# Optimization experiments

Measured on AMD Instinct MI355X. Metric: run time of the kernel, lower is better.

## Reference

```python
import jax, jax.numpy as jnp
import numpy as np

B, T, N, DIN, HID, ED, K = 64, 12, 1024, 2, 64, 10, 2

def setup_inputs() -> dict:
    key = jax.random.key(0)
    ks = jax.random.split(key, 18)
    g = lambda i, shape, s=0.1: jax.random.normal(ks[i], shape, jnp.float32) * s
    return dict(
        x=g(0, (B, T, N, DIN), 1.0),
        node_embeddings=g(1, (N, ED), 1.0),
        # GCRN cell 0 (dim_in=DIN): gate -> 2*HID, update -> HID
        Wg0=g(2, (ED, K, DIN + HID, 2 * HID)), bg0=g(3, (ED, 2 * HID)),
        Wu0=g(4, (ED, K, DIN + HID, HID)),     bu0=g(5, (ED, HID)),
        # GCRN cell 1 (dim_in=HID)
        Wg1=g(6, (ED, K, 2 * HID, 2 * HID)),   bg1=g(7, (ED, 2 * HID)),
        Wu1=g(8, (ED, K, 2 * HID, HID)),       bu1=g(9, (ED, HID)),
        # RelatinoShipConv: pointwise Linear(input_dim -> rnn_units), torch [out,in]
        Wr=g(10, (HID, DIN)), br=g(11, (HID,)),
        # end_conv1: Linear(HID,HID, bias=False) (num_layers>1 branch)
        W1=g(12, (HID, HID)),
        # self.conv: Conv2d(horizon, horizon, (1, HID+1), bias=False), OIHW
        Wc=g(13, (T, T, 1, HID + 1)),
        # end_conv2: Conv2d(horizon, horizon, (1, HID), bias)
        W2=g(14, (T, T, 1, HID)), b2=g(15, (T,)),
        # end_conv3: Conv2d(horizon, horizon, (1, 2), dilation (1, HID), bias)
        W3=g(16, (T, T, 1, 2)), b3=g(17, (T,)),
    )

def _avwgcn(x, supports, E, Wp, bp):
    # x:[B,N,C], supports:[K,N,N], E:[N,ED] -> [B,N,O]  (AGCRN adaptive graph conv)
    xg = jnp.einsum('knm,bmc->bnkc', supports, x)
    W = jnp.einsum('ne,ekio->nkio', E, Wp)
    b = E @ bp
    return jnp.einsum('bnki,nkio->bno', xg, W) + b

def _cell(xt, h, supports, E, Wg, bg, Wu, bu):
    # GCRN GRU cell
    zr = jax.nn.sigmoid(_avwgcn(jnp.concatenate([xt, h], -1), supports, E, Wg, bg))
    z, r = jnp.split(zr, 2, -1)
    hc = jnp.tanh(_avwgcn(jnp.concatenate([xt, z * h], -1), supports, E, Wu, bu))
    return r * h + (1.0 - r) * hc

def _conv2d(x, w, b=None, rhs_dilation=(1, 1)):
    y = jax.lax.conv_general_dilated(x, w, (1, 1), 'VALID',
        rhs_dilation=rhs_dilation, dimension_numbers=('NCHW', 'OIHW', 'NCHW'))
    return y if b is None else y + b[None, :, None, None]

def _forward(x, E, Wg0, bg0, Wu0, bu0, Wg1, bg1, Wu1, bu1, Wr, br, W1, Wc, W2, b2, W3, b3):
    A = jax.nn.softmax(jax.nn.relu(E @ E.T), axis=1)
    supports = jnp.stack([jnp.eye(N, dtype=x.dtype), A], 0)  # [K,N,N]
    # GCRN encoder: python loop over 2 layers, lax.scan over the 12 timesteps
    cur = x
    for (Wg, bg, Wu, bu) in ((Wg0, bg0, Wu0, bu0), (Wg1, bg1, Wu1, bu1)):
        h0 = jnp.zeros((x.shape[0], N, HID), x.dtype)
        def step(h, xt):
            h = _cell(xt, h, supports, E, Wg, bg, Wu, bu)
            return h, h
        _, hs = jax.lax.scan(step, h0, jnp.swapaxes(cur, 0, 1))
        cur = jnp.swapaxes(hs, 0, 1)  # [B,T,N,HID]
    out = cur @ W1.T  # end_conv1 (Linear, no bias); dropout is identity in eval
    relation = x @ Wr.T + br  # [B,T,N,HID]
    # torch einsum 'btnc,knn->kbcnt' takes the DIAGONAL of supports over n
    rg = jnp.einsum('btnc,knn->kbcnt', relation, supports)
    rg = jnp.transpose(rg, (1, 4, 3, 2, 0)).reshape(x.shape[0], T, N, -1)  # [B,12,N,2*HID]
    rst = _conv2d(rg, Wc)  # [B,12,N,HID]
    out = _conv2d(jnp.concatenate([rst, out], -1), W2, b2)  # [B,12,N,HID+1]
    out = _conv2d(out, W3, b3, rhs_dilation=(1, HID))       # [B,12,N,1]
    return out

def reference(x, node_embeddings, Wg0, bg0, Wu0, bu0, Wg1, bg1, Wu1, bu1, Wr, br, W1, Wc, W2, b2, W3, b3):
    return _forward(x, node_embeddings, Wg0, bg0, Wu0, bu0, Wg1, bg1, Wu1, bu1, Wr, br, W1, Wc, W2, b2, W3, b3)
```

## Files before the change

kernel.cpp:

```cpp
#include <hip/hip_runtime.h>

typedef unsigned short u16;
typedef unsigned int   u32;

__device__ __forceinline__ float bf2f(u16 u){ return __uint_as_float(((u32)u)<<16); }
__device__ __forceinline__ u16 f2bf(float f){
  u32 u = __float_as_uint(f);
  return (u16)((u + 0x7fffu + ((u>>16)&1u)) >> 16);
}

__global__ __launch_bounds__(256) void k_A2(const float* __restrict__ E,
    float* __restrict__ A, float* __restrict__ diagA)
{
  __shared__ float EL[10][1024];
  __shared__ float row[1024];
  __shared__ float red[4];
  int n = blockIdx.x, tid = threadIdx.x;
  for (int idx=tid; idx<10240; idx+=256)
    EL[idx>>10][idx&1023] = E[(idx&1023)*10 + (idx>>10)];
  __syncthreads();
  float en[10];
#pragma unroll
  for (int e=0;e<10;++e) en[e] = EL[e][n];
  float lmax = -1e30f;
#pragma unroll
  for (int j=0;j<4;++j){
    int m = tid*4 + j;
    float d = 0.f;
#pragma unroll
    for (int e=0;e<10;++e) d = fmaf(en[e], EL[e][m], d);
    d = fmaxf(d, 0.f);
    row[m] = d; lmax = fmaxf(lmax, d);
  }
#pragma unroll
  for (int o=32;o>0;o>>=1) lmax = fmaxf(lmax, __shfl_xor(lmax, o));
  if ((tid&63)==0) red[tid>>6] = lmax;
  __syncthreads();
  float mx = fmaxf(fmaxf(red[0],red[1]), fmaxf(red[2],red[3]));
  __syncthreads();
  float lsum = 0.f;
#pragma unroll
  for (int j=0;j<4;++j){
    int m = tid*4 + j;
    float ex = expf(row[m] - mx);
    row[m] = ex; lsum += ex;
  }
#pragma unroll
  for (int o=32;o>0;o>>=1) lsum += __shfl_xor(lsum, o);
  if ((tid&63)==0) red[tid>>6] = lsum;
  __syncthreads();
  float inv = 1.f/(red[0]+red[1]+red[2]+red[3]);
#pragma unroll
  for (int j=0;j<4;++j){
    int m = tid*4 + j;
    float v = row[m]*inv;
    A[(size_t)n*1024 + m] = v;
    if (m == n) diagA[n] = v;
  }
}

__global__ __launch_bounds__(64) void k_b3eff(
    const float* __restrict__ b2, const float* __restrict__ W3,
    const float* __restrict__ b3, float* __restrict__ b3eff)
{
  int o = threadIdx.x;
  if (o < 12){
    float a = b3[o];
    for (int i=0;i<12;++i)
      a += b2[i] * (W3[(o*12+i)*2] + W3[(o*12+i)*2+1]);
    b3eff[o] = a;
  }
}

__global__ __launch_bounds__(256) void k_Vpre(const float* __restrict__ W1,
    const float* __restrict__ W2, float* __restrict__ V)
{
  int idx = blockIdx.x*256 + threadIdx.x;
  if (idx >= 9216) return;
  int c = idx & 63, r = idx >> 6;
  int j = r % 12, i = r / 12;
  float a = 0.f;
  for (int o=0;o<64;++o)
    a = fmaf(W2[(i*12+j)*64+o], W1[o*64+c], a);
  V[idx] = a;
}

__global__ __launch_bounds__(256) void k_Gpre(const float* __restrict__ Wc,
    const float* __restrict__ W2, u16* __restrict__ G)
{
  int idx = blockIdx.x*256 + threadIdx.x;
  int u = idx & 127, r = idx >> 7;
  int ip = r % 12, i = r / 12;
  float a = 0.f;
  int wlo = u>64 ? u-64 : 0;
  int whi = u<63 ? u : 63;
  for (int j=0;j<12;++j){
    const float* w2r = W2 + (i*12+j)*64;
    const float* wcr = Wc + (j*12+ip)*65;
    for (int w=wlo; w<=whi; ++w)
      a = fmaf(w2r[w], wcr[u-w], a);
  }
  G[idx] = f2bf(a);
}

__global__ __launch_bounds__(256) void gemm3f(const float* __restrict__ A,
    const float* __restrict__ X, float* __restrict__ Y)
{
  int n0 = blockIdx.x * 128;
  long base = (long)blockIdx.y * 65536;
  __shared__ float At[16][132];
  __shared__ float Xt[16][64];
  int tid = threadIdx.x;
  int tx = tid & 15, ty = tid >> 4;
  float acc[8][4];
#pragma unroll
  for (int r=0;r<8;++r){ acc[r][0]=0;acc[r][1]=0;acc[r][2]=0;acc[r][3]=0; }

  for (int m0=0; m0<1024; m0+=16){
    {
      int r = tid>>1, kh = (tid&1)*8;
      const float* ap = A + (size_t)(n0+r)*1024 + m0 + kh;
      float4 q0 = *(const float4*)ap;
      float4 q1 = *(const float4*)(ap+4);
      At[kh+0][r]=q0.x; At[kh+1][r]=q0.y; At[kh+2][r]=q0.z; At[kh+3][r]=q0.w;
      At[kh+4][r]=q1.x; At[kh+5][r]=q1.y; At[kh+6][r]=q1.z; At[kh+7][r]=q1.w;
    }
    {
      int c = tid & 63, kq = tid >> 6;
#pragma unroll
      for (int j=0;j<4;++j)
        Xt[kq*4+j][c] = X[base + (long)(m0+kq*4+j)*64 + c];
    }
    __syncthreads();
#pragma unroll
    for (int kk=0;kk<16;++kk){
      float4 xv = *(const float4*)&Xt[kk][tx*4];
      float4 a0 = *(const float4*)&At[kk][ty*4];
      float4 a1 = *(const float4*)&At[kk][64+ty*4];
      float av[8] = {a0.x,a0.y,a0.z,a0.w,a1.x,a1.y,a1.z,a1.w};
      float xw[4] = {xv.x,xv.y,xv.z,xv.w};
#pragma unroll
      for (int r=0;r<8;++r)
#pragma unroll
        for (int c=0;c<4;++c) acc[r][c] = fmaf(av[r], xw[c], acc[r][c]);
    }
    __syncthreads();
  }
#pragma unroll
  for (int half=0; half<2; ++half)
#pragma unroll
    for (int i=0;i<4;++i){
      int row = n0 + half*64 + ty*4 + i;
      float4 v; v.x=acc[half*4+i][0]; v.y=acc[half*4+i][1];
      v.z=acc[half*4+i][2]; v.w=acc[half*4+i][3];
      *(float4*)&Y[base + (long)row*64 + tx*4] = v;
    }
}

__global__ __launch_bounds__(256) void gemm2x(const float* __restrict__ A,
    const float* __restrict__ x, float* __restrict__ Y)
{
  __shared__ float As[64][65];
  __shared__ float Xs[64][65];
  int n0 = blockIdx.x*64;
  int q0 = blockIdx.y*64;
  int tid = threadIdx.x, c = tid & 63, rq = tid >> 6;
  float acc[16];
#pragma unroll
  for (int j=0;j<16;++j) acc[j]=0.f;
  for (int m0=0; m0<1024; m0+=64){
#pragma unroll
    for (int j=0;j<16;++j){
      int idx = tid + j*256;
      int r = idx>>6, k = idx&63;
      As[r][k] = A[(size_t)(n0+r)*1024 + m0 + k];
      int qg = q0 + k;
      Xs[r][k] = x[(size_t)(qg>>1)*2048 + (size_t)(m0+r)*2 + (qg&1)];
    }
    __syncthreads();
    for (int k=0;k<64;++k){
      float xv = Xs[k][c];
#pragma unroll
      for (int j=0;j<16;++j) acc[j] = fmaf(As[rq+4*j][k], xv, acc[j]);
    }
    __syncthreads();
  }
#pragma unroll
  for (int j=0;j<16;++j)
    Y[(size_t)(n0+rq+4*j)*1536 + q0 + c] = acc[j];
}

template<int L>
__global__ __launch_bounds__(256) void k_gate2(
    const float* __restrict__ Wg, const float* __restrict__ bgp,
    const float* __restrict__ E,
    const float* __restrict__ xsrc, const float* __restrict__ Axt,
    const float* __restrict__ h, const float* __restrict__ Ah,
    float* __restrict__ zh, float* __restrict__ rb, int t, int first)
{
  constexpr int IX  = (L==0)?2:64;
  constexpr int KI  = 2*(IX+64);
  constexpr int CH  = (L==0)?44:32;
  constexpr int NCH = KI/CH;
  constexpr int O   = 128;
  __shared__ float inp[32][KI];
  __shared__ float Wl[CH][O];
  __shared__ float En[10];
  int n = blockIdx.x, b0 = blockIdx.y*32, tid = threadIdx.x;

  if (tid < 10) En[tid] = E[n*10 + tid];
  for (int idx=tid; idx<32*IX; idx+=256){
    int bl = idx/IX, i = idx - bl*IX; int b = b0+bl;
    inp[bl][i] = (L==0)
      ? xsrc[(size_t)((b*12+t)*1024+n)*2 + i]
      : xsrc[((size_t)b<<16) + (size_t)n*64 + i];
  }
  for (int idx=tid; idx<2048; idx+=256){
    int bl = idx>>6, c = idx&63; int b = b0+bl;
    inp[bl][IX+c] = first ? 0.f : h[((size_t)b<<16) + (size_t)n*64 + c];
  }
  for (int idx=tid; idx<32*IX; idx+=256){
    int bl = idx/IX, i = idx - bl*IX; int b = b0+bl;
    inp[bl][IX+64+i] = (L==0)
      ? Axt[(size_t)n*1536 + (size_t)(b*12+t)*2 + i]
      : Axt[((size_t)b<<16) + (size_t)n*64 + i];
  }
  for (int idx=tid; idx<2048; idx+=256){
    int bl = idx>>6, c = idx&63; int b = b0+bl;
    inp[bl][2*IX+64+c] = first ? 0.f : Ah[((size_t)b<<16) + (size_t)n*64 + c];
  }
  __syncthreads();

  int bg = tid >> 5;
  int og = tid & 31;
  float acc[4][4];
#pragma unroll
  for (int d=0;d<4;++d){
    int o = og*4+d;
    float a = 0.f;
#pragma unroll
    for (int e=0;e<10;++e) a = fmaf(En[e], bgp[e*O+o], a);
#pragma unroll
    for (int bl=0;bl<4;++bl) acc[bl][d] = a;
  }

  for (int ch=0; ch<NCH; ++ch){
    for (int idx=tid; idx<CH*O; idx+=256){
      int i = idx>>7, o = idx&127;
      float a = 0.f;
#pragma unroll
      for (int e=0;e<10;++e)
        a = fmaf(En[e], Wg[((size_t)e*KI + ch*CH + i)*O + o], a);
      Wl[i][o] = a;
    }
    __syncthreads();
    for (int i=0; i<CH; i+=4){
      float4 xq[4], wq[4];
#pragma unroll
      for (int bl=0;bl<4;++bl) xq[bl] = *(const float4*)&inp[bg*4+bl][ch*CH+i];
#pragma unroll
      for (int ii=0;ii<4;++ii) wq[ii] = *(const float4*)&Wl[i+ii][og*4];
      float xv[4][4], wv[4][4];
#pragma unroll
      for (int bl=0;bl<4;++bl){ xv[bl][0]=xq[bl].x; xv[bl][1]=xq[bl].y; xv[bl][2]=xq[bl].z; xv[bl][3]=xq[bl].w; }
#pragma unroll
      for (int ii=0;ii<4;++ii){ wv[ii][0]=wq[ii].x; wv[ii][1]=wq[ii].y; wv[ii][2]=wq[ii].z; wv[ii][3]=wq[ii].w; }
#pragma unroll
      for (int bl=0;bl<4;++bl)
#pragma unroll
        for (int d=0;d<4;++d)
#pragma unroll
          for (int ii=0;ii<4;++ii)
            acc[bl][d] = fmaf(xv[bl][ii], wv[ii][d], acc[bl][d]);
    }
    __syncthreads();
  }

#pragma unroll
  for (int bl=0;bl<4;++bl){
    int b = b0 + bg*4 + bl;
    size_t base = ((size_t)b<<16) + (size_t)n*64;
#pragma unroll
    for (int d=0;d<4;++d){
      int o = og*4 + d;
      float s = 1.f/(1.f+__expf(-acc[bl][d]));
      if (o < 64){
        if (!first) zh[base+o] = s * h[base+o];
      } else {
        rb[base+o-64] = s;
      }
    }
  }
}

template<int L>
__global__ __launch_bounds__(256) void k_upd2(
    const float* __restrict__ Wu, const float* __restrict__ bup,
    const float* __restrict__ E,
    const float* __restrict__ xsrc, const float* __restrict__ Axt,
    const float* __restrict__ zh, const float* __restrict__ Azh,
    const float* __restrict__ rb, float* __restrict__ h, int t, int first)
{
  constexpr int IX  = (L==0)?2:64;
  constexpr int KI  = 2*(IX+64);
  constexpr int CH  = (L==0)?44:64;
  constexpr int NCH = KI/CH;
  constexpr int O   = 64;
  __shared__ float inp[32][KI];
  __shared__ float Wl[CH][O];
  __shared__ float En[10];
  int n = blockIdx.x, b0 = blockIdx.y*32, tid = threadIdx.x;

  if (tid < 10) En[tid] = E[n*10 + tid];
  for (int idx=tid; idx<32*IX; idx+=256){
    int bl = idx/IX, i = idx - bl*IX; int b = b0+bl;
    inp[bl][i] = (L==0)
      ? xsrc[(size_t)((b*12+t)*1024+n)*2 + i]
      : xsrc[((size_t)b<<16) + (size_t)n*64 + i];
  }
  for (int idx=tid; idx<2048; idx+=256){
    int bl = idx>>6, c = idx&63; int b = b0+bl;
    inp[bl][IX+c] = first ? 0.f : zh[((size_t)b<<16) + (size_t)n*64 + c];
  }
  for (int idx=tid; idx<32*IX; idx+=256){
    int bl = idx/IX, i = idx - bl*IX; int b = b0+bl;
    inp[bl][IX+64+i] = (L==0)
      ? Axt[(size_t)n*1536 + (size_t)(b*12+t)*2 + i]
      : Axt[((size_t)b<<16) + (size_t)n*64 + i];
  }
  for (int idx=tid; idx<2048; idx+=256){
    int bl = idx>>6, c = idx&63; int b = b0+bl;
    inp[bl][2*IX+64+c] = first ? 0.f : Azh[((size_t)b<<16) + (size_t)n*64 + c];
  }
  __syncthreads();

  int bg = tid >> 5;
  int og = tid & 31;
  float acc[4][2];
#pragma unroll
  for (int d=0;d<2;++d){
    int o = og*2+d;
    float a = 0.f;
#pragma unroll
    for (int e=0;e<10;++e) a = fmaf(En[e], bup[e*O+o], a);
#pragma unroll
    for (int bl=0;bl<4;++bl) acc[bl][d] = a;
  }

  for (int ch=0; ch<NCH; ++ch){
    for (int idx=tid; idx<CH*O; idx+=256){
      int i = idx>>6, o = idx&63;
      float a = 0.f;
#pragma unroll
      for (int e=0;e<10;++e)
        a = fmaf(En[e], Wu[((size_t)e*KI + ch*CH + i)*O + o], a);
      Wl[i][o] = a;
    }
    __syncthreads();
    for (int i=0; i<CH; i+=4){
      float4 xq[4]; float2 wq[4];
#pragma unroll
      for (int bl=0;bl<4;++bl) xq[bl] = *(const float4*)&inp[bg*4+bl][ch*CH+i];
#pragma unroll
      for (int ii=0;ii<4;++ii) wq[ii] = *(const float2*)&Wl[i+ii][og*2];
      float xv[4][4], wv[4][2];
#pragma unroll
      for (int bl=0;bl<4;++bl){ xv[bl][0]=xq[bl].x; xv[bl][1]=xq[bl].y; xv[bl][2]=xq[bl].z; xv[bl][3]=xq[bl].w; }
#pragma unroll
      for (int ii=0;ii<4;++ii){ wv[ii][0]=wq[ii].x; wv[ii][1]=wq[ii].y; }
#pragma unroll
      for (int bl=0;bl<4;++bl)
#pragma unroll
        for (int d=0;d<2;++d)
#pragma unroll
          for (int ii=0;ii<4;++ii)
            acc[bl][d] = fmaf(xv[bl][ii], wv[ii][d], acc[bl][d]);
    }
    __syncthreads();
  }

#pragma unroll
  for (int bl=0;bl<4;++bl){
    int b = b0 + bg*4 + bl;
    size_t base = ((size_t)b<<16) + (size_t)n*64;
#pragma unroll
    for (int d=0;d<2;++d){
      int o = og*2 + d;
      float hc = tanhf(acc[bl][d]);
      float r  = rb[base+o];
      float h0v = first ? 0.f : h[base+o];
      h[base+o] = r*h0v + (1.f-r)*hc;
    }
  }
}

__global__ __launch_bounds__(256) void k_q1t(const float* __restrict__ h1,
    const float* __restrict__ V, float* __restrict__ q1acc, int t, int first)
{
  __shared__ float VL[12][64];
  int n = blockIdx.x, tid = threadIdx.x;
  for (int idx=tid; idx<768; idx+=256){
    int i = idx>>6, c = idx&63;
    VL[i][c] = V[(i*12+t)*64 + c];
  }
  __syncthreads();
  for (int task=tid; task<768; task+=256){
    int b = task/12, i = task - (task/12)*12;
    const float* hv = h1 + ((size_t)b<<16) + (size_t)n*64;
    float s = 0.f;
#pragma unroll
    for (int c=0;c<64;++c) s = fmaf(hv[c], VL[i][c], s);
    size_t qi = (((size_t)b<<10) + n)*12 + i;
    if (first) q1acc[qi] = s; else q1acc[qi] += s;
  }
}

__global__ __launch_bounds__(256) void k_q0G(
    const float* __restrict__ x, const float* __restrict__ diagA,
    const u16* __restrict__ G,
    const float* __restrict__ Wr, const float* __restrict__ br,
    float* __restrict__ q0buf)
{
  int n = blockIdx.x, tid = threadIdx.x;
  __shared__ u16  GL[18432];
  __shared__ float xsL[64][24];
  __shared__ float WrL[64][2];
  __shared__ float brL[64];

  for (int idx=tid; idx<18432; idx+=256) GL[idx] = G[idx];
  for (int idx=tid; idx<1536; idx+=256){
    int b = idx/24, r = idx - b*24;
    xsL[b][r] = x[(size_t)((b*12+(r>>1))*1024+n)*2 + (r&1)];
  }
  if (tid<128) WrL[tid>>1][tid&1] = Wr[tid];
  else if (tid<192) brL[tid-128] = br[tid-128];
  __syncthreads();

  float dA = diagA[n];
  int b = tid & 63, iq = tid >> 6;
  int i0 = iq*3;
  float q0a=0.f, q0b=0.f, q0c=0.f;
  for (int ip=0; ip<12; ++ip){
    float xa = xsL[b][ip*2], xb = xsL[b][ip*2+1];
    const u16* g0r = &GL[((i0+0)*12+ip)*128];
    const u16* g1r = &GL[((i0+1)*12+ip)*128];
    const u16* g2r = &GL[((i0+2)*12+ip)*128];
    for (int c=0;c<64;++c){
      float rel  = fmaf(xa, WrL[c][0], fmaf(xb, WrL[c][1], brL[c]));
      float relD = rel * dA;
      u32 g0 = *(const u32*)&g0r[2*c];
      u32 g1 = *(const u32*)&g1r[2*c];
      u32 g2 = *(const u32*)&g2r[2*c];
      q0a = fmaf(rel, bf2f((u16)g0), fmaf(relD, bf2f((u16)(g0>>16)), q0a));
      q0b = fmaf(rel, bf2f((u16)g1), fmaf(relD, bf2f((u16)(g1>>16)), q0b));
      q0c = fmaf(rel, bf2f((u16)g2), fmaf(relD, bf2f((u16)(g2>>16)), q0c));
    }
  }
  size_t qb = (((size_t)b<<10) + n)*12;
  q0buf[qb+i0]   = q0a;
  q0buf[qb+i0+1] = q0b;
  q0buf[qb+i0+2] = q0c;
}

__global__ __launch_bounds__(256) void k_head2(
    const float* __restrict__ q0buf, const float* __restrict__ q1acc,
    const float* __restrict__ W3, const float* __restrict__ b3eff,
    float* __restrict__ out)
{
  int n = blockIdx.x, tid = threadIdx.x;
  __shared__ float W3L[12][12][2];
  __shared__ float b3eL[12];
  __shared__ float q0L[64][12];
  __shared__ float q1L[64][12];

  if (tid < 12) b3eL[tid] = b3eff[tid];
  for (int idx=tid; idx<288; idx+=256){
    int o = idx/24, r = idx - o*24;
    W3L[o][r>>1][r&1] = W3[idx];
  }
  for (int idx=tid; idx<768; idx+=256){
    int b = idx/12, i = idx - (idx/12)*12;
    size_t base = (((size_t)b<<10) + n)*12 + i;
    q0L[b][i] = q0buf[base];
    q1L[b][i] = q1acc[base];
  }
  __syncthreads();

  for (int idx=tid; idx<768; idx+=256){
    int bb = idx/12, o = idx - (idx/12)*12;
    float a = b3eL[o];
#pragma unroll
    for (int i=0;i<12;++i)
      a += q0L[bb][i]*W3L[o][i][0] + q1L[bb][i]*W3L[o][i][1];
    out[(size_t)(bb*12+o)*1024 + n] = a;
  }
}

extern "C" void kernel_launch(void* const* d_in, const int* in_sizes, int n_in,
                              void* d_out, int out_size, void* d_ws, size_t ws_size,
                              hipStream_t stream)
{
  const float* x   = (const float*)d_in[0];
  const float* E   = (const float*)d_in[1];
  const float* Wg0 = (const float*)d_in[2];
  const float* bg0 = (const float*)d_in[3];
  const float* Wu0 = (const float*)d_in[4];
  const float* bu0 = (const float*)d_in[5];
  const float* Wg1 = (const float*)d_in[6];
  const float* bg1 = (const float*)d_in[7];
  const float* Wu1 = (const float*)d_in[8];
  const float* bu1 = (const float*)d_in[9];
  const float* Wr  = (const float*)d_in[10];
  const float* br  = (const float*)d_in[11];
  const float* W1  = (const float*)d_in[12];
  const float* Wc  = (const float*)d_in[13];
  const float* W2  = (const float*)d_in[14];
  const float* b2  = (const float*)d_in[15];
  const float* W3  = (const float*)d_in[16];
  const float* b3  = (const float*)d_in[17];

  char* ws = (char*)d_ws;
  size_t off = 0;
  auto alloc = [&](size_t bytes)->void*{
    void* p = ws + off; off += (bytes + 255) & ~(size_t)255; return p;
  };
  float* A     = (float*)alloc(1024ull*1024*4);
  float* diagA = (float*)alloc(1024*4);
  float* Ax0T  = (float*)alloc(1024ull*1536*4);
  float* AhZ0  = (float*)alloc(64ull*65536*4);
  float* AhZ1  = (float*)alloc(64ull*65536*4);
  float* zh    = (float*)alloc(64ull*65536*4);
  float* rb    = (float*)alloc(64ull*65536*4);
  float* Axt1  = (float*)alloc(64ull*65536*4);
  float* h0    = (float*)alloc(64ull*65536*4);
  float* h1    = (float*)alloc(64ull*65536*4);
  float* q1acc = (float*)alloc(64ull*1024*12*4);
  float* q0buf = (float*)alloc(64ull*1024*12*4);
  float* V     = (float*)alloc(12ull*12*64*4);
  u16*   G     = (u16*)alloc(12ull*12*128*2);
  float* b3eff = (float*)alloc(12*4);

  if (off > ws_size) return;

  k_A2<<<dim3(1024),256,0,stream>>>(E, A, diagA);
  k_b3eff<<<dim3(1),64,0,stream>>>(b2, W3, b3, b3eff);
  k_Vpre<<<dim3(36),256,0,stream>>>(W1, W2, V);
  k_Gpre<<<dim3(72),256,0,stream>>>(Wc, W2, G);
  gemm2x<<<dim3(16,24),256,0,stream>>>(A, x, Ax0T);
  k_q0G<<<dim3(1024),256,0,stream>>>(x, diagA, G, Wr, br, q0buf);

  for (int t=0;t<12;++t){
    int first = (t==0);
    k_gate2<0><<<dim3(1024,2),256,0,stream>>>(Wg0, bg0, E, x, Ax0T, h0, Axt1,
                                              zh, rb, t, first);
    if (!first) gemm3f<<<dim3(8,64),256,0,stream>>>(A, zh, AhZ0);
    k_upd2<0><<<dim3(1024,2),256,0,stream>>>(Wu0, bu0, E, x, Ax0T, zh, AhZ0,
                                             rb, h0, t, first);
    gemm3f<<<dim3(8,64),256,0,stream>>>(A, h0, Axt1);
    if (!first) gemm3f<<<dim3(8,64),256,0,stream>>>(A, h1, AhZ1);
    k_gate2<1><<<dim3(1024,2),256,0,stream>>>(Wg1, bg1, E, h0, Axt1, h1, AhZ1,
                                              zh, rb, t, first);
    if (!first) gemm3f<<<dim3(8,64),256,0,stream>>>(A, zh, AhZ0);
    k_upd2<1><<<dim3(1024,2),256,0,stream>>>(Wu1, bu1, E, h0, Axt1, zh, AhZ0,
                                             rb, h1, t, first);
    k_q1t<<<dim3(1024),256,0,stream>>>(h1, V, q1acc, t, first);
  }

  k_head2<<<dim3(1024),256,0,stream>>>(q0buf, q1acc, W3, b3eff, (float*)d_out);
}
```

Measured before the change: 10.79 ms.

## Precompute transposed adjacency, widen GEMM k-tile, batch two graph GEMMs per launch

The softmax adjacency kernel now also writes a transposed copy of A. The graph-propagation GEMM reads that copy with coalesced float4 loads straight into shared memory, with no transposing scatter, and processes 32 k-rows per tile instead of 16, which halves the number of barriers. The two independent A·h0 and A·h1 products are merged into a single launch using blockIdx.z. A small shared-array padding change is also included. The cost is an extra 4 MB buffer, one extra strided write pass in the setup kernel, and larger shared-memory tiles.

```diff
diff --git a/kernel.cpp b/kernel.cpp
--- a/kernel.cpp
+++ b/kernel.cpp
@@ -10,7 +10,7 @@
 }
 
 __global__ __launch_bounds__(256) void k_A2(const float* __restrict__ E,
-    float* __restrict__ A, float* __restrict__ diagA)
+    float* __restrict__ A, float* __restrict__ At, float* __restrict__ diagA)
 {
   __shared__ float EL[10][1024];
   __shared__ float row[1024];
@@ -54,7 +54,8 @@
   for (int j=0;j<4;++j){
     int m = tid*4 + j;
     float v = row[m]*inv;
-    A[(size_t)n*1024 + m] = v;
+    A[(size_t)n*1024 + m]  = v;
+    At[(size_t)m*1024 + n] = v;
     if (m == n) diagA[n] = v;
   }
 }
@@ -103,40 +104,42 @@
   G[idx] = f2bf(a);
 }
 
-__global__ __launch_bounds__(256) void gemm3f(const float* __restrict__ A,
-    const float* __restrict__ X, float* __restrict__ Y)
-{
+__global__ __launch_bounds__(256) void gemm4(const float* __restrict__ At,
+    const float* __restrict__ X0, float* __restrict__ Y0,
+    const float* __restrict__ X1, float* __restrict__ Y1)
+{
+  const float* X = blockIdx.z ? X1 : X0;
+  float*       Y = blockIdx.z ? Y1 : Y0;
   int n0 = blockIdx.x * 128;
   long base = (long)blockIdx.y * 65536;
-  __shared__ float At[16][132];
-  __shared__ float Xt[16][64];
+  __shared__ float Al[32*128];
+  __shared__ float Xl[32*64];
   int tid = threadIdx.x;
   int tx = tid & 15, ty = tid >> 4;
   float acc[8][4];
 #pragma unroll
   for (int r=0;r<8;++r){ acc[r][0]=0;acc[r][1]=0;acc[r][2]=0;acc[r][3]=0; }
 
-  for (int m0=0; m0<1024; m0+=16){
-    {
-      int r = tid>>1, kh = (tid&1)*8;
-      const float* ap = A + (size_t)(n0+r)*1024 + m0 + kh;
-      float4 q0 = *(const float4*)ap;
-      float4 q1 = *(const float4*)(ap+4);
-      At[kh+0][r]=q0.x; At[kh+1][r]=q0.y; At[kh+2][r]=q0.z; At[kh+3][r]=q0.w;
-      At[kh+4][r]=q1.x; At[kh+5][r]=q1.y; At[kh+6][r]=q1.z; At[kh+7][r]=q1.w;
-    }
-    {
-      int c = tid & 63, kq = tid >> 6;
-#pragma unroll
-      for (int j=0;j<4;++j)
-        Xt[kq*4+j][c] = X[base + (long)(m0+kq*4+j)*64 + c];
-    }
-    __syncthreads();
-#pragma unroll
-    for (int kk=0;kk<16;++kk){
-      float4 xv = *(const float4*)&Xt[kk][tx*4];
-      float4 a0 = *(const float4*)&At[kk][ty*4];
-      float4 a1 = *(const float4*)&At[kk][64+ty*4];
+  for (int m0=0; m0<1024; m0+=32){
+#pragma unroll
+    for (int i=0;i<4;++i){
+      int fo = tid + i*256;
+      int k = fo >> 5, nl4 = fo & 31;
+      float4 v = *(const float4*)(At + (size_t)(m0+k)*1024 + n0 + nl4*4);
+      *(float4*)(Al + fo*4) = v;
+    }
+#pragma unroll
+    for (int i=0;i<2;++i){
+      int fo = tid + i*256;
+      float4 v = *(const float4*)(X + base + (long)m0*64 + fo*4);
+      *(float4*)(Xl + fo*4) = v;
+    }
+    __syncthreads();
+#pragma unroll
+    for (int kk=0;kk<32;++kk){
+      float4 xv = *(const float4*)(Xl + kk*64 + tx*4);
+      float4 a0 = *(const float4*)(Al + kk*128 + ty*4);
+      float4 a1 = *(const float4*)(Al + kk*128 + 64 + ty*4);
       float av[8] = {a0.x,a0.y,a0.z,a0.w,a1.x,a1.y,a1.z,a1.w};
       float xw[4] = {xv.x,xv.y,xv.z,xv.w};
 #pragma unroll
@@ -423,7 +426,7 @@
 {
   int n = blockIdx.x, tid = threadIdx.x;
   __shared__ u16  GL[18432];
-  __shared__ float xsL[64][24];
+  __shared__ float xsL[64][25];
   __shared__ float WrL[64][2];
   __shared__ float brL[64];
 
@@ -525,6 +528,7 @@
     void* p = ws + off; off += (bytes + 255) & ~(size_t)255; return p;
   };
   float* A     = (float*)alloc(1024ull*1024*4);
+  float* At    = (float*)alloc(1024ull*1024*4);
   float* diagA = (float*)alloc(1024*4);
   float* Ax0T  = (float*)alloc(1024ull*1536*4);
   float* AhZ0  = (float*)alloc(64ull*65536*4);
@@ -542,7 +546,7 @@
 
   if (off > ws_size) return;
 
-  k_A2<<<dim3(1024),256,0,stream>>>(E, A, diagA);
+  k_A2<<<dim3(1024),256,0,stream>>>(E, A, At, diagA);
   k_b3eff<<<dim3(1),64,0,stream>>>(b2, W3, b3, b3eff);
   k_Vpre<<<dim3(36),256,0,stream>>>(W1, W2, V);
   k_Gpre<<<dim3(72),256,0,stream>>>(Wc, W2, G);
@@ -553,14 +557,13 @@
     int first = (t==0);
     k_gate2<0><<<dim3(1024,2),256,0,stream>>>(Wg0, bg0, E, x, Ax0T, h0, Axt1,
                                               zh, rb, t, first);
-    if (!first) gemm3f<<<dim3(8,64),256,0,stream>>>(A, zh, AhZ0);
+    if (!first) gemm4<<<dim3(8,64,1),256,0,stream>>>(At, zh, AhZ0, nullptr, nullptr);
     k_upd2<0><<<dim3(1024,2),256,0,stream>>>(Wu0, bu0, E, x, Ax0T, zh, AhZ0,
                                              rb, h0, t, first);
-    gemm3f<<<dim3(8,64),256,0,stream>>>(A, h0, Axt1);
-    if (!first) gemm3f<<<dim3(8,64),256,0,stream>>>(A, h1, AhZ1);
+    gemm4<<<dim3(8,64, first?1:2),256,0,stream>>>(At, h0, Axt1, h1, AhZ1);
     k_gate2<1><<<dim3(1024,2),256,0,stream>>>(Wg1, bg1, E, h0, Axt1, h1, AhZ1,
                                               zh, rb, t, first);
-    if (!first) gemm3f<<<dim3(8,64),256,0,stream>>>(A, zh, AhZ0);
+    if (!first) gemm4<<<dim3(8,64,1),256,0,stream>>>(At, zh, AhZ0, nullptr, nullptr);
     k_upd2<1><<<dim3(1024,2),256,0,stream>>>(Wu1, bu1, E, h0, Axt1, zh, AhZ0,
                                              rb, h1, t, first);
     k_q1t<<<dim3(1024),256,0,stream>>>(h1, V, q1acc, t, first);
```

New measurement: 10.48 ms. -2.9%, faster.
